# Kernel tuning notes

Measured on AMD Instinct MI355X. Metric: run time of the kernel, lower is better.

## Reference

```python
import jax, jax.numpy as jnp
import numpy as np

EPS = 1e-8


def setup_inputs() -> dict:
    key = jax.random.key(0)
    k1, k2, k3, k4, k5 = jax.random.split(key, 5)
    B, N_LOG, N_PHYS, E = 16, 512, 2048, 2048
    P = jax.random.uniform(k1, (B, N_LOG, N_PHYS), dtype=jnp.float32)
    d_hw = jax.random.randint(k2, (N_PHYS, N_PHYS), 0, 4, dtype=jnp.int32)
    edge_src = jax.random.randint(k3, (B, E), 0, N_LOG, dtype=jnp.int32)
    edge_dst = jax.random.randint(k4, (B, E), 0, N_LOG, dtype=jnp.int32)
    edge_w = jax.random.uniform(k5, (B, E), dtype=jnp.float32)
    return {"P": P, "d_hw": d_hw, "edge_src": edge_src,
            "edge_dst": edge_dst, "edge_w": edge_w}


def reference(P, d_hw, edge_src, edge_dst, edge_w):
    # A_hw[p,q] = 1 where hardware distance == 1 (adjacent qubits)
    A_hw = (d_hw == 1).astype(P.dtype)                      # [Q, Q]
    B = P.shape[0]
    # Dense contraction once per batch: PA[b,i,q] = sum_p P[b,i,p] A[p,q]
    PA = jnp.einsum('bip,pq->biq', P, A_hw)                 # [B, N, Q]
    b_idx = jnp.arange(B)[:, None]                          # [B, 1]
    gi = PA[b_idx, edge_src]                                # [B, E, Q]
    gj = P[b_idx, edge_dst]                                 # [B, E, Q]
    adj_score = jnp.einsum('beq,beq->be', gi, gj)           # [B, E]
    sample_adj = jnp.sum(edge_w * adj_score, axis=-1)       # [B]
    sample_weight = jnp.maximum(jnp.sum(edge_w, axis=-1), EPS)
    # every sample has edges -> valid_samples = B
    loss = -jnp.mean(sample_adj / sample_weight)
    return loss
```

## Files before the change

kernel.cpp:

```cpp
#include <hip/hip_runtime.h>
#include <hip/hip_bf16.h>

#define BATCH 16
#define NLOG 512
#define Q 2048
#define NEDGE 2048
#define M_TOT (BATCH * NLOG)
#define KB 2048

typedef float f32x4 __attribute__((ext_vector_type(4)));
typedef int i32x4 __attribute__((ext_vector_type(4)));
typedef int i32x8 __attribute__((ext_vector_type(8)));

__device__ __forceinline__ unsigned char to_e4m3(float f) {
    int pk = __builtin_amdgcn_cvt_pk_fp8_f32(f, f, 0, false);
    return (unsigned char)(pk & 0xff);
}

__global__ __launch_bounds__(256) void prep(const float* __restrict__ P,
                                            unsigned char* __restrict__ P8,
                                            const int* __restrict__ d_hw,
                                            unsigned char* __restrict__ A8t,
                                            unsigned* __restrict__ counter) {
    int bid = blockIdx.x;
    if (bid == 0 && threadIdx.x == 0) *counter = 0u;
    if (bid < 8192) {
        int i = (bid * 256 + threadIdx.x) * 8;
        float4 v0 = *(const float4*)(P + i);
        float4 v1 = *(const float4*)(P + i + 4);
        int lo = 0, hi = 0;
        lo = __builtin_amdgcn_cvt_pk_fp8_f32(v0.x, v0.y, lo, false);
        lo = __builtin_amdgcn_cvt_pk_fp8_f32(v0.z, v0.w, lo, true);
        hi = __builtin_amdgcn_cvt_pk_fp8_f32(v1.x, v1.y, hi, false);
        hi = __builtin_amdgcn_cvt_pk_fp8_f32(v1.z, v1.w, hi, true);
        int2 st; st.x = lo; st.y = hi;
        *(int2*)(P8 + i) = st;
    } else {
        bid -= 8192;
        __shared__ unsigned char tile[32][33];
        int q0 = (bid & 63) * 32;
        int p0 = (bid >> 6) * 32;
        int tx = threadIdx.x & 31;
        int ty = threadIdx.x >> 5;
        for (int s = 0; s < 32; s += 8) {
            int p = p0 + ty + s;
            int v = d_hw[(size_t)p * Q + q0 + tx];
            tile[ty + s][tx] = (v == 1) ? 0x38 : 0x00;
        }
        __syncthreads();
        for (int s = 0; s < 32; s += 8) {
            A8t[(size_t)(q0 + ty + s) * Q + p0 + tx] = tile[tx][ty + s];
        }
    }
}

__global__ __launch_bounds__(256, 2) void gemm_bt8(const unsigned char* __restrict__ A,
                                                   const unsigned char* __restrict__ Bt,
                                                   unsigned char* __restrict__ PA8) {
    __shared__ unsigned char As[32768];
    __shared__ unsigned char Bs[16384];

    const int t = threadIdx.x;
    const int w = t >> 6;
    const int wr = w >> 1, wc = w & 1;
    const int l = t & 63;
    const int quad = l >> 4;
    const int lane16 = l & 15;

    const int m0 = blockIdx.x * 256;
    const int n0 = blockIdx.y * 128;

    const int s_row = t >> 3;
    const int s_off = (((t & 7) ^ (s_row & 7)) << 4);

    const int r7 = lane16 & 7;
    const int c0 = ((2 * quad) ^ r7) << 4;
    const int c1 = ((2 * quad + 1) ^ r7) << 4;

    f32x4 acc[8][4] = {};

    for (int k0 = 0; k0 < KB; k0 += 128) {
        #pragma unroll
        for (int c = 0; c < 8; c++) {
            const unsigned char* g = A + (size_t)(m0 + c * 32 + s_row) * KB + k0 + s_off;
            __builtin_amdgcn_global_load_lds(
                (const __attribute__((address_space(1))) void*)g,
                (__attribute__((address_space(3))) void*)(As + c * 4096 + w * 1024),
                16, 0, 0);
        }
        #pragma unroll
        for (int c = 0; c < 4; c++) {
            const unsigned char* g = Bt + (size_t)(n0 + c * 32 + s_row) * KB + k0 + s_off;
            __builtin_amdgcn_global_load_lds(
                (const __attribute__((address_space(1))) void*)g,
                (__attribute__((address_space(3))) void*)(Bs + c * 4096 + w * 1024),
                16, 0, 0);
        }
        __syncthreads();

        i32x8 bfr[4];
        #pragma unroll
        for (int j = 0; j < 4; j++) {
            int base = (wc * 64 + j * 16 + lane16) << 7;
            i32x4 lo = *(const i32x4*)(Bs + base + c0);
            i32x4 hi = *(const i32x4*)(Bs + base + c1);
            bfr[j] = __builtin_shufflevector(lo, hi, 0, 1, 2, 3, 4, 5, 6, 7);
        }
        #pragma unroll
        for (int i = 0; i < 8; i++) {
            int base = (wr * 128 + i * 16 + lane16) << 7;
            i32x4 lo = *(const i32x4*)(As + base + c0);
            i32x4 hi = *(const i32x4*)(As + base + c1);
            i32x8 af = __builtin_shufflevector(lo, hi, 0, 1, 2, 3, 4, 5, 6, 7);
            #pragma unroll
            for (int j = 0; j < 4; j++)
                acc[i][j] = __builtin_amdgcn_mfma_scale_f32_16x16x128_f8f6f4(
                    af, bfr[j], acc[i][j], 0, 0,
                    0, 127,
                    0, 127);
        }
        __syncthreads();
    }

    #pragma unroll
    for (int i = 0; i < 8; i++) {
        #pragma unroll
        for (int j = 0; j < 4; j++) {
            #pragma unroll
            for (int r = 0; r < 4; r++) {
                int row = m0 + wr * 128 + i * 16 + quad * 4 + r;
                int col = n0 + wc * 64 + j * 16 + lane16;
                PA8[(size_t)row * Q + col] = to_e4m3(acc[i][j][r] * (1.0f / 256.0f));
            }
        }
    }
}

__global__ __launch_bounds__(256, 2) void gemm_s8(const unsigned char* __restrict__ PA8,
                                                  const unsigned char* __restrict__ P8,
                                                  __hip_bfloat16* __restrict__ S) {
    __shared__ unsigned char As[8192];
    __shared__ unsigned char Bs[16384];

    const int t = threadIdx.x;
    const int w = t >> 6;
    const int wr = w >> 1, wc = w & 1;
    const int l = t & 63;
    const int quad = l >> 4;
    const int lane16 = l & 15;

    const int b = blockIdx.z;
    const int m0 = blockIdx.x * 64;
    const int n0 = blockIdx.y * 128;
    const unsigned char* A  = PA8 + (size_t)b * NLOG * Q;
    const unsigned char* Bt = P8  + (size_t)b * NLOG * Q;
    __hip_bfloat16* C = S + (size_t)b * NLOG * NLOG;

    const int s_row = t >> 3;
    const int s_off = (((t & 7) ^ (s_row & 7)) << 4);
    const int r7 = lane16 & 7;
    const int c0 = ((2 * quad) ^ r7) << 4;
    const int c1 = ((2 * quad + 1) ^ r7) << 4;

    f32x4 acc[2][4] = {};

    for (int k0 = 0; k0 < KB; k0 += 128) {
        #pragma unroll
        for (int c = 0; c < 2; c++) {
            const unsigned char* g = A + (size_t)(m0 + c * 32 + s_row) * KB + k0 + s_off;
            __builtin_amdgcn_global_load_lds(
                (const __attribute__((address_space(1))) void*)g,
                (__attribute__((address_space(3))) void*)(As + c * 4096 + w * 1024),
                16, 0, 0);
        }
        #pragma unroll
        for (int c = 0; c < 4; c++) {
            const unsigned char* g = Bt + (size_t)(n0 + c * 32 + s_row) * KB + k0 + s_off;
            __builtin_amdgcn_global_load_lds(
                (const __attribute__((address_space(1))) void*)g,
                (__attribute__((address_space(3))) void*)(Bs + c * 4096 + w * 1024),
                16, 0, 0);
        }
        __syncthreads();

        i32x8 bfr[4];
        #pragma unroll
        for (int j = 0; j < 4; j++) {
            int base = (wc * 64 + j * 16 + lane16) << 7;
            i32x4 lo = *(const i32x4*)(Bs + base + c0);
            i32x4 hi = *(const i32x4*)(Bs + base + c1);
            bfr[j] = __builtin_shufflevector(lo, hi, 0, 1, 2, 3, 4, 5, 6, 7);
        }
        #pragma unroll
        for (int i = 0; i < 2; i++) {
            int base = (wr * 32 + i * 16 + lane16) << 7;
            i32x4 lo = *(const i32x4*)(As + base + c0);
            i32x4 hi = *(const i32x4*)(As + base + c1);
            i32x8 af = __builtin_shufflevector(lo, hi, 0, 1, 2, 3, 4, 5, 6, 7);
            #pragma unroll
            for (int j = 0; j < 4; j++)
                acc[i][j] = __builtin_amdgcn_mfma_scale_f32_16x16x128_f8f6f4(
                    af, bfr[j], acc[i][j], 0, 0, 0, 127, 0, 127);
        }
        __syncthreads();
    }

    #pragma unroll
    for (int i = 0; i < 2; i++) {
        #pragma unroll
        for (int j = 0; j < 4; j++) {
            #pragma unroll
            for (int r = 0; r < 4; r++) {
                int row = m0 + wr * 32 + i * 16 + quad * 4 + r;
                int col = n0 + wc * 64 + j * 16 + lane16;
                C[(size_t)row * NLOG + col] = __float2bfloat16(acc[i][j][r]);
            }
        }
    }
}

__global__ __launch_bounds__(256) void edge_final(const __hip_bfloat16* __restrict__ S,
                                                  const int* __restrict__ esrc,
                                                  const int* __restrict__ edst,
                                                  const float* __restrict__ ew,
                                                  float* __restrict__ adj,
                                                  float* __restrict__ wsum,
                                                  unsigned* __restrict__ counter,
                                                  float* __restrict__ out) {
    const int b = blockIdx.x;
    const int t = threadIdx.x;
    const unsigned short* Sb = (const unsigned short*)S + (size_t)b * NLOG * NLOG;
    float a = 0.f, ws = 0.f;
    #pragma unroll
    for (int k = 0; k < NEDGE / 256; k++) {
        int e = b * NEDGE + k * 256 + t;
        int src = esrc[e];
        int dst = edst[e];
        float wg = ew[e];
        float s = __uint_as_float((unsigned)Sb[src * NLOG + dst] << 16) * 256.0f;
        a += wg * s;
        ws += wg;
    }
    #pragma unroll
    for (int off = 32; off > 0; off >>= 1) {
        a += __shfl_xor(a, off);
        ws += __shfl_xor(ws, off);
    }
    __shared__ float ra[4], rw[4];
    if ((t & 63) == 0) { ra[t >> 6] = a; rw[t >> 6] = ws; }
    __syncthreads();

    __shared__ unsigned done;
    if (t == 0) {
        atomicExch(&adj[b],  ra[0] + ra[1] + ra[2] + ra[3]);
        atomicExch(&wsum[b], rw[0] + rw[1] + rw[2] + rw[3]);
        __threadfence();
        done = atomicAdd(counter, 1u);
    }
    __syncthreads();
    if (done == BATCH - 1 && t == 0) {
        __threadfence();
        float s = 0.f;
        #pragma unroll
        for (int bb = 0; bb < BATCH; bb++) {
            float av = atomicAdd(&adj[bb], 0.0f);
            float wv = atomicAdd(&wsum[bb], 0.0f);
            s += av / fmaxf(wv, 1e-8f);
        }
        out[0] = -s / (float)BATCH;
    }
}

extern "C" void kernel_launch(void* const* d_in, const int* in_sizes, int n_in,
                              void* d_out, int out_size, void* d_ws, size_t ws_size,
                              hipStream_t stream) {
    const float* P    = (const float*)d_in[0];
    const int* d_hw   = (const int*)d_in[1];
    const int* esrc   = (const int*)d_in[2];
    const int* edst   = (const int*)d_in[3];
    const float* ew   = (const float*)d_in[4];
    float* out        = (float*)d_out;

    char* ws = (char*)d_ws;
    unsigned char* P8  = (unsigned char*)ws;
    unsigned char* A8t = (unsigned char*)(ws + 16777216);
    unsigned char* PA8 = (unsigned char*)(ws + 20971520);
    __hip_bfloat16* S  = (__hip_bfloat16*)(ws + 37748736);
    float* adj         = (float*)(ws + 46137344);
    float* wsum        = (float*)(ws + 46137344 + 64);
    unsigned* counter  = (unsigned*)(ws + 46137344 + 128);

    prep<<<8192 + 4096, 256, 0, stream>>>(P, P8, d_hw, A8t, counter);
    gemm_bt8<<<dim3(M_TOT / 256, Q / 128), 256, 0, stream>>>(P8, A8t, PA8);
    gemm_s8<<<dim3(NLOG / 64, NLOG / 128, BATCH), 256, 0, stream>>>(PA8, P8, S);
    edge_final<<<BATCH, 256, 0, stream>>>(S, esrc, edst, ew, adj, wsum, counter, out);
}
```

Before: 181.4 us.

## Reassociate loss as masked P^T W P contraction with scattered edge weights

Scatters edge weights into a dense per-batch W matrix, computes V = P^T W P over the batch-concatenated K dimension, and reduces V against a bitmask of adjacent hardware pairs. This replaces the P·A GEMM plus per-sample S GEMM and edge gather. The per-sample weight normalization is folded into the gemm1 epilogue. It adds fp8 quantization of W and of the scaled intermediate, which can cost accuracy, and it performs an fp8 transpose of P in prep.

```diff
diff --git a/kernel.cpp b/kernel.cpp
--- a/kernel.cpp
+++ b/kernel.cpp
@@ -5,8 +5,7 @@
 #define NLOG 512
 #define Q 2048
 #define NEDGE 2048
-#define M_TOT (BATCH * NLOG)
-#define KB 2048
+#define KTOT 8192
 
 typedef float f32x4 __attribute__((ext_vector_type(4)));
 typedef int i32x4 __attribute__((ext_vector_type(4)));
@@ -18,45 +17,90 @@
 }
 
 __global__ __launch_bounds__(256) void prep(const float* __restrict__ P,
-                                            unsigned char* __restrict__ P8,
+                                            unsigned char* __restrict__ P8t,
                                             const int* __restrict__ d_hw,
-                                            unsigned char* __restrict__ A8t,
+                                            unsigned* __restrict__ mask,
+                                            const float* __restrict__ ew,
+                                            float* __restrict__ sw,
+                                            float* __restrict__ total,
                                             unsigned* __restrict__ counter) {
+    const int t = threadIdx.x;
     int bid = blockIdx.x;
-    if (bid == 0 && threadIdx.x == 0) *counter = 0u;
-    if (bid < 8192) {
-        int i = (bid * 256 + threadIdx.x) * 8;
-        float4 v0 = *(const float4*)(P + i);
-        float4 v1 = *(const float4*)(P + i + 4);
-        int lo = 0, hi = 0;
-        lo = __builtin_amdgcn_cvt_pk_fp8_f32(v0.x, v0.y, lo, false);
-        lo = __builtin_amdgcn_cvt_pk_fp8_f32(v0.z, v0.w, lo, true);
-        hi = __builtin_amdgcn_cvt_pk_fp8_f32(v1.x, v1.y, hi, false);
-        hi = __builtin_amdgcn_cvt_pk_fp8_f32(v1.z, v1.w, hi, true);
-        int2 st; st.x = lo; st.y = hi;
-        *(int2*)(P8 + i) = st;
+    if (bid < 16384) {
+        __shared__ unsigned char tile[32][36];
+        const int b = bid >> 10;
+        const int tb = bid & 1023;
+        const int i0 = (tb >> 6) * 32;
+        const int p0 = (tb & 63) * 32;
+        const int tx = t & 31, ty = t >> 5;
+        #pragma unroll
+        for (int s = 0; s < 4; s++) {
+            int r = ty + s * 8;
+            float v = P[(size_t)(b * NLOG + i0 + r) * Q + p0 + tx];
+            tile[r][tx] = to_e4m3(v);
+        }
+        __syncthreads();
+        const int r2 = t >> 3;
+        const int c4 = (t & 7) * 4;
+        uchar4 o;
+        o.x = tile[c4 + 0][r2];
+        o.y = tile[c4 + 1][r2];
+        o.z = tile[c4 + 2][r2];
+        o.w = tile[c4 + 3][r2];
+        *(uchar4*)(P8t + (size_t)(p0 + r2) * KTOT + b * NLOG + i0 + c4) = o;
+    } else if (bid < 16896) {
+        int wordid = (bid - 16384) * 256 + t;
+        int p = wordid >> 6;
+        int qw = wordid & 63;
+        unsigned m = 0;
+        #pragma unroll
+        for (int u = 0; u < 32; u++) {
+            int d = d_hw[(size_t)p * Q + qw * 32 + u];
+            m |= (unsigned)(d == 1) << u;
+        }
+        mask[wordid] = m;
     } else {
-        bid -= 8192;
-        __shared__ unsigned char tile[32][33];
-        int q0 = (bid & 63) * 32;
-        int p0 = (bid >> 6) * 32;
-        int tx = threadIdx.x & 31;
-        int ty = threadIdx.x >> 5;
-        for (int s = 0; s < 32; s += 8) {
-            int p = p0 + ty + s;
-            int v = d_hw[(size_t)p * Q + q0 + tx];
-            tile[ty + s][tx] = (v == 1) ? 0x38 : 0x00;
-        }
-        __syncthreads();
-        for (int s = 0; s < 32; s += 8) {
-            A8t[(size_t)(q0 + ty + s) * Q + p0 + tx] = tile[tx][ty + s];
-        }
-    }
-}
-
-__global__ __launch_bounds__(256, 2) void gemm_bt8(const unsigned char* __restrict__ A,
-                                                   const unsigned char* __restrict__ Bt,
-                                                   unsigned char* __restrict__ PA8) {
+        int b = bid - 16896;
+        if (b == 0 && t == 0) { *total = 0.f; *counter = 0u; }
+        float s = 0.f;
+        #pragma unroll
+        for (int k = 0; k < 8; k++) s += ew[b * NEDGE + k * 256 + t];
+        #pragma unroll
+        for (int off = 32; off > 0; off >>= 1) s += __shfl_xor(s, off);
+        __shared__ float red[4];
+        if ((t & 63) == 0) red[t >> 6] = s;
+        __syncthreads();
+        if (t == 0) sw[b] = red[0] + red[1] + red[2] + red[3];
+    }
+}
+
+__global__ __launch_bounds__(256) void scatter_w(const int* __restrict__ esrc,
+                                                 const int* __restrict__ edst,
+                                                 const float* __restrict__ ew,
+                                                 float* __restrict__ Wf32) {
+    const int b = blockIdx.x;
+    const int t = threadIdx.x;
+    #pragma unroll
+    for (int s = 0; s < 8; s++) {
+        int e = b * NEDGE + s * 256 + t;
+        atomicAdd(&Wf32[(size_t)b * NLOG * NLOG + esrc[e] * NLOG + edst[e]], ew[e]);
+    }
+}
+
+__global__ __launch_bounds__(256) void cvt_w(const float* __restrict__ Wf32,
+                                             unsigned char* __restrict__ W8) {
+    int i = (blockIdx.x * 256 + threadIdx.x) * 4;
+    float4 v = *(const float4*)(Wf32 + i);
+    int pk = 0;
+    pk = __builtin_amdgcn_cvt_pk_fp8_f32(v.x, v.y, pk, false);
+    pk = __builtin_amdgcn_cvt_pk_fp8_f32(v.z, v.w, pk, true);
+    *(int*)(W8 + i) = pk;
+}
+
+__global__ __launch_bounds__(256, 2) void gemm1(const unsigned char* __restrict__ P8t,
+                                                const unsigned char* __restrict__ W8,
+                                                const float* __restrict__ sw,
+                                                unsigned char* __restrict__ Vt) {
     __shared__ unsigned char As[32768];
     __shared__ unsigned char Bs[16384];
 
@@ -67,22 +111,25 @@
     const int quad = l >> 4;
     const int lane16 = l & 15;
 
+    const int b = blockIdx.z;
     const int m0 = blockIdx.x * 256;
     const int n0 = blockIdx.y * 128;
 
     const int s_row = t >> 3;
     const int s_off = (((t & 7) ^ (s_row & 7)) << 4);
-
     const int r7 = lane16 & 7;
     const int c0 = ((2 * quad) ^ r7) << 4;
     const int c1 = ((2 * quad + 1) ^ r7) << 4;
 
+    const unsigned char* Wb = W8 + (size_t)b * NLOG * NLOG;
+
     f32x4 acc[8][4] = {};
 
-    for (int k0 = 0; k0 < KB; k0 += 128) {
+    for (int k0 = 0; k0 < NLOG; k0 += 128) {
         #pragma unroll
         for (int c = 0; c < 8; c++) {
-            const unsigned char* g = A + (size_t)(m0 + c * 32 + s_row) * KB + k0 + s_off;
+            const unsigned char* g = P8t + (size_t)(m0 + c * 32 + s_row) * KTOT
+                                     + b * NLOG + k0 + s_off;
             __builtin_amdgcn_global_load_lds(
                 (const __attribute__((address_space(1))) void*)g,
                 (__attribute__((address_space(3))) void*)(As + c * 4096 + w * 1024),
@@ -90,7 +137,8 @@
         }
         #pragma unroll
         for (int c = 0; c < 4; c++) {
-            const unsigned char* g = Bt + (size_t)(n0 + c * 32 + s_row) * KB + k0 + s_off;
+            const unsigned char* g = Wb + (size_t)(n0 + c * 32 + s_row) * NLOG
+                                     + k0 + s_off;
             __builtin_amdgcn_global_load_lds(
                 (const __attribute__((address_space(1))) void*)g,
                 (__attribute__((address_space(3))) void*)(Bs + c * 4096 + w * 1024),
@@ -115,31 +163,41 @@
             #pragma unroll
             for (int j = 0; j < 4; j++)
                 acc[i][j] = __builtin_amdgcn_mfma_scale_f32_16x16x128_f8f6f4(
-                    af, bfr[j], acc[i][j], 0, 0,
-                    0, 127,
-                    0, 127);
-        }
-        __syncthreads();
-    }
-
-    #pragma unroll
-    for (int i = 0; i < 8; i++) {
-        #pragma unroll
-        for (int j = 0; j < 4; j++) {
+                    af, bfr[j], acc[i][j], 0, 0, 0, 127, 0, 127);
+        }
+        __syncthreads();
+    }
+
+    const float scale = 1024.0f / fmaxf(sw[b], 1e-8f);
+    unsigned char* Cs = As;
+    #pragma unroll
+    for (int i = 0; i < 8; i++)
+        #pragma unroll
+        for (int j = 0; j < 4; j++)
             #pragma unroll
             for (int r = 0; r < 4; r++) {
-                int row = m0 + wr * 128 + i * 16 + quad * 4 + r;
-                int col = n0 + wc * 64 + j * 16 + lane16;
-                PA8[(size_t)row * Q + col] = to_e4m3(acc[i][j][r] * (1.0f / 256.0f));
+                int row = wr * 128 + i * 16 + quad * 4 + r;
+                int col = wc * 64 + j * 16 + lane16;
+                Cs[row * 128 + col] = to_e4m3(acc[i][j][r] * scale);
             }
-        }
-    }
-}
-
-__global__ __launch_bounds__(256, 2) void gemm_s8(const unsigned char* __restrict__ PA8,
-                                                  const unsigned char* __restrict__ P8,
-                                                  __hip_bfloat16* __restrict__ S) {
-    __shared__ unsigned char As[8192];
+    __syncthreads();
+    #pragma unroll
+    for (int s = 0; s < 8; s++) {
+        int idx = s * 4096 + t * 16;
+        int row = idx >> 7;
+        int col = idx & 127;
+        *(i32x4*)(Vt + (size_t)(m0 + row) * KTOT + b * NLOG + n0 + col) =
+            *(const i32x4*)(Cs + idx);
+    }
+}
+
+__global__ __launch_bounds__(256, 2) void gemm2(const unsigned char* __restrict__ P8t,
+                                                const unsigned char* __restrict__ Vt,
+                                                const unsigned* __restrict__ mask,
+                                                float* __restrict__ total,
+                                                unsigned* __restrict__ counter,
+                                                float* __restrict__ out) {
+    __shared__ unsigned char As[32768];
     __shared__ unsigned char Bs[16384];
 
     const int t = threadIdx.x;
@@ -149,12 +207,9 @@
     const int quad = l >> 4;
     const int lane16 = l & 15;
 
-    const int b = blockIdx.z;
-    const int m0 = blockIdx.x * 64;
+    const int m0 = blockIdx.x * 256;
     const int n0 = blockIdx.y * 128;
-    const unsigned char* A  = PA8 + (size_t)b * NLOG * Q;
-    const unsigned char* Bt = P8  + (size_t)b * NLOG * Q;
-    __hip_bfloat16* C = S + (size_t)b * NLOG * NLOG;
+    const int kbase = blockIdx.z * 2048;
 
     const int s_row = t >> 3;
     const int s_off = (((t & 7) ^ (s_row & 7)) << 4);
@@ -162,12 +217,13 @@
     const int c0 = ((2 * quad) ^ r7) << 4;
     const int c1 = ((2 * quad + 1) ^ r7) << 4;
 
-    f32x4 acc[2][4] = {};
-
-    for (int k0 = 0; k0 < KB; k0 += 128) {
-        #pragma unroll
-        for (int c = 0; c < 2; c++) {
-            const unsigned char* g = A + (size_t)(m0 + c * 32 + s_row) * KB + k0 + s_off;
+    f32x4 acc[8][4] = {};
+
+    for (int k0 = 0; k0 < 2048; k0 += 128) {
+        #pragma unroll
+        for (int c = 0; c < 8; c++) {
+            const unsigned char* g = P8t + (size_t)(m0 + c * 32 + s_row) * KTOT
+                                     + kbase + k0 + s_off;
             __builtin_amdgcn_global_load_lds(
                 (const __attribute__((address_space(1))) void*)g,
                 (__attribute__((address_space(3))) void*)(As + c * 4096 + w * 1024),
@@ -175,7 +231,8 @@
         }
         #pragma unroll
         for (int c = 0; c < 4; c++) {
-            const unsigned char* g = Bt + (size_t)(n0 + c * 32 + s_row) * KB + k0 + s_off;
+            const unsigned char* g = Vt + (size_t)(n0 + c * 32 + s_row) * KTOT
+                                     + kbase + k0 + s_off;
             __builtin_amdgcn_global_load_lds(
                 (const __attribute__((address_space(1))) void*)g,
                 (__attribute__((address_space(3))) void*)(Bs + c * 4096 + w * 1024),
@@ -192,8 +249,8 @@
             bfr[j] = __builtin_shufflevector(lo, hi, 0, 1, 2, 3, 4, 5, 6, 7);
         }
         #pragma unroll
-        for (int i = 0; i < 2; i++) {
-            int base = (wr * 32 + i * 16 + lane16) << 7;
+        for (int i = 0; i < 8; i++) {
+            int base = (wr * 128 + i * 16 + lane16) << 7;
             i32x4 lo = *(const i32x4*)(As + base + c0);
             i32x4 hi = *(const i32x4*)(As + base + c1);
             i32x8 af = __builtin_shufflevector(lo, hi, 0, 1, 2, 3, 4, 5, 6, 7);
@@ -205,69 +262,37 @@
         __syncthreads();
     }
 
-    #pragma unroll
-    for (int i = 0; i < 2; i++) {
-        #pragma unroll
-        for (int j = 0; j < 4; j++) {
+    float part = 0.f;
+    #pragma unroll
+    for (int i = 0; i < 8; i++) {
+        #pragma unroll
+        for (int r = 0; r < 4; r++) {
+            int p = m0 + wr * 128 + i * 16 + quad * 4 + r;
             #pragma unroll
-            for (int r = 0; r < 4; r++) {
-                int row = m0 + wr * 32 + i * 16 + quad * 4 + r;
-                int col = n0 + wc * 64 + j * 16 + lane16;
-                C[(size_t)row * NLOG + col] = __float2bfloat16(acc[i][j][r]);
+            for (int j = 0; j < 4; j++) {
+                int q = n0 + wc * 64 + j * 16 + lane16;
+                unsigned mw = mask[p * (Q / 32) + (q >> 5)];
+                if ((mw >> (q & 31)) & 1u) part += acc[i][j][r];
             }
         }
     }
-}
-
-__global__ __launch_bounds__(256) void edge_final(const __hip_bfloat16* __restrict__ S,
-                                                  const int* __restrict__ esrc,
-                                                  const int* __restrict__ edst,
-                                                  const float* __restrict__ ew,
-                                                  float* __restrict__ adj,
-                                                  float* __restrict__ wsum,
-                                                  unsigned* __restrict__ counter,
-                                                  float* __restrict__ out) {
-    const int b = blockIdx.x;
-    const int t = threadIdx.x;
-    const unsigned short* Sb = (const unsigned short*)S + (size_t)b * NLOG * NLOG;
-    float a = 0.f, ws = 0.f;
-    #pragma unroll
-    for (int k = 0; k < NEDGE / 256; k++) {
-        int e = b * NEDGE + k * 256 + t;
-        int src = esrc[e];
-        int dst = edst[e];
-        float wg = ew[e];
-        float s = __uint_as_float((unsigned)Sb[src * NLOG + dst] << 16) * 256.0f;
-        a += wg * s;
-        ws += wg;
-    }
-    #pragma unroll
-    for (int off = 32; off > 0; off >>= 1) {
-        a += __shfl_xor(a, off);
-        ws += __shfl_xor(ws, off);
-    }
-    __shared__ float ra[4], rw[4];
-    if ((t & 63) == 0) { ra[t >> 6] = a; rw[t >> 6] = ws; }
+    #pragma unroll
+    for (int off = 32; off > 0; off >>= 1) part += __shfl_xor(part, off);
+    __shared__ float red[4];
+    if (l == 0) red[w] = part;
     __syncthreads();
 
     __shared__ unsigned done;
     if (t == 0) {
-        atomicExch(&adj[b],  ra[0] + ra[1] + ra[2] + ra[3]);
-        atomicExch(&wsum[b], rw[0] + rw[1] + rw[2] + rw[3]);
+        atomicAdd(total, red[0] + red[1] + red[2] + red[3]);
         __threadfence();
         done = atomicAdd(counter, 1u);
     }
     __syncthreads();
-    if (done == BATCH - 1 && t == 0) {
+    if (t == 0 && done == 8 * 16 * 4 - 1) {
         __threadfence();
-        float s = 0.f;
-        #pragma unroll
-        for (int bb = 0; bb < BATCH; bb++) {
-            float av = atomicAdd(&adj[bb], 0.0f);
-            float wv = atomicAdd(&wsum[bb], 0.0f);
-            s += av / fmaxf(wv, 1e-8f);
-        }
-        out[0] = -s / (float)BATCH;
+        float tv = atomicAdd(total, 0.0f);
+        out[0] = -tv / 16384.0f;
     }
 }
 
@@ -282,16 +307,21 @@
     float* out        = (float*)d_out;
 
     char* ws = (char*)d_ws;
-    unsigned char* P8  = (unsigned char*)ws;
-    unsigned char* A8t = (unsigned char*)(ws + 16777216);
-    unsigned char* PA8 = (unsigned char*)(ws + 20971520);
-    __hip_bfloat16* S  = (__hip_bfloat16*)(ws + 37748736);
-    float* adj         = (float*)(ws + 46137344);
-    float* wsum        = (float*)(ws + 46137344 + 64);
-    unsigned* counter  = (unsigned*)(ws + 46137344 + 128);
-
-    prep<<<8192 + 4096, 256, 0, stream>>>(P, P8, d_hw, A8t, counter);
-    gemm_bt8<<<dim3(M_TOT / 256, Q / 128), 256, 0, stream>>>(P8, A8t, PA8);
-    gemm_s8<<<dim3(NLOG / 64, NLOG / 128, BATCH), 256, 0, stream>>>(PA8, P8, S);
-    edge_final<<<BATCH, 256, 0, stream>>>(S, esrc, edst, ew, adj, wsum, counter, out);
-}
+    unsigned char* P8t = (unsigned char*)ws;
+    unsigned char* W8  = (unsigned char*)(ws + 16777216);
+    float* Wf32        = (float*)(ws + 20971520);
+    unsigned char* Vt  = (unsigned char*)(ws + 20971520);
+    unsigned* mask     = (unsigned*)(ws + 37748736);
+    float* sw          = (float*)(ws + 38273024);
+    float* total       = (float*)(ws + 38273088);
+    unsigned* counter  = (unsigned*)(ws + 38273152);
+
+    hipMemsetAsync(Wf32, 0, 16777216, stream);
+    prep<<<16384 + 512 + 16, 256, 0, stream>>>(P, P8t, d_hw, mask, ew, sw,
+                                               total, counter);
+    scatter_w<<<BATCH, 256, 0, stream>>>(esrc, edst, ew, Wf32);
+    cvt_w<<<4096, 256, 0, stream>>>(Wf32, W8);
+    gemm1<<<dim3(Q / 256, NLOG / 128, BATCH), 256, 0, stream>>>(P8t, W8, sw, Vt);
+    gemm2<<<dim3(Q / 256, Q / 128, 4), 256, 0, stream>>>(P8t, Vt, mask, total,
+                                                         counter, out);
+}
```

After: 188.2 us. 3.7% more time.

## Fuse edge reduction into S GEMM epilogue via scattered dense edge-weight matrix

Applied to the files above, without the earlier changes.

Edge weights are scattered with atomics into a dense per-batch fp32 weight matrix during prep, along with per-batch weight sums. The second GEMM then multiplies its accumulators by the matching weight entries and reduces straight into a global total, so the bf16 S matrix write and the separate edge_final kernel go away. The cost is a 16 MB memset, 16 MB of fp32 weight reads in the GEMM epilogue, and atomics on a single total scalar. It also drops the bf16 rounding of S.

```diff
diff --git a/kernel.cpp b/kernel.cpp
--- a/kernel.cpp
+++ b/kernel.cpp
@@ -21,11 +21,17 @@
                                             unsigned char* __restrict__ P8,
                                             const int* __restrict__ d_hw,
                                             unsigned char* __restrict__ A8t,
+                                            const int* __restrict__ esrc,
+                                            const int* __restrict__ edst,
+                                            const float* __restrict__ ew,
+                                            float* __restrict__ Wf32,
+                                            float* __restrict__ sw,
+                                            float* __restrict__ total,
                                             unsigned* __restrict__ counter) {
+    const int t = threadIdx.x;
     int bid = blockIdx.x;
-    if (bid == 0 && threadIdx.x == 0) *counter = 0u;
     if (bid < 8192) {
-        int i = (bid * 256 + threadIdx.x) * 8;
+        int i = (bid * 256 + t) * 8;
         float4 v0 = *(const float4*)(P + i);
         float4 v1 = *(const float4*)(P + i + 4);
         int lo = 0, hi = 0;
@@ -35,13 +41,13 @@
         hi = __builtin_amdgcn_cvt_pk_fp8_f32(v1.z, v1.w, hi, true);
         int2 st; st.x = lo; st.y = hi;
         *(int2*)(P8 + i) = st;
-    } else {
+    } else if (bid < 12288) {
         bid -= 8192;
         __shared__ unsigned char tile[32][33];
         int q0 = (bid & 63) * 32;
         int p0 = (bid >> 6) * 32;
-        int tx = threadIdx.x & 31;
-        int ty = threadIdx.x >> 5;
+        int tx = t & 31;
+        int ty = t >> 5;
         for (int s = 0; s < 32; s += 8) {
             int p = p0 + ty + s;
             int v = d_hw[(size_t)p * Q + q0 + tx];
@@ -51,6 +57,24 @@
         for (int s = 0; s < 32; s += 8) {
             A8t[(size_t)(q0 + ty + s) * Q + p0 + tx] = tile[tx][ty + s];
         }
+    } else {
+        int b = bid - 12288;
+        if (b == 0 && t == 0) { *total = 0.f; *counter = 0u; }
+        float s = 0.f;
+        float* Wb = Wf32 + (size_t)b * NLOG * NLOG;
+        #pragma unroll
+        for (int k = 0; k < 8; k++) {
+            int e = b * NEDGE + k * 256 + t;
+            float wg = ew[e];
+            s += wg;
+            atomicAdd(&Wb[esrc[e] * NLOG + edst[e]], wg);
+        }
+        #pragma unroll
+        for (int off = 32; off > 0; off >>= 1) s += __shfl_xor(s, off);
+        __shared__ float red[4];
+        if ((t & 63) == 0) red[t >> 6] = s;
+        __syncthreads();
+        if (t == 0) sw[b] = red[0] + red[1] + red[2] + red[3];
     }
 }
 
@@ -72,7 +96,6 @@
 
     const int s_row = t >> 3;
     const int s_off = (((t & 7) ^ (s_row & 7)) << 4);
-
     const int r7 = lane16 & 7;
     const int c0 = ((2 * quad) ^ r7) << 4;
     const int c1 = ((2 * quad + 1) ^ r7) << 4;
@@ -115,9 +138,7 @@
             #pragma unroll
             for (int j = 0; j < 4; j++)
                 acc[i][j] = __builtin_amdgcn_mfma_scale_f32_16x16x128_f8f6f4(
-                    af, bfr[j], acc[i][j], 0, 0,
-                    0, 127,
-                    0, 127);
+                    af, bfr[j], acc[i][j], 0, 0, 0, 127, 0, 127);
         }
         __syncthreads();
     }
@@ -136,9 +157,13 @@
     }
 }
 
-__global__ __launch_bounds__(256, 2) void gemm_s8(const unsigned char* __restrict__ PA8,
+__global__ __launch_bounds__(256, 2) void gemm_sw(const unsigned char* __restrict__ PA8,
                                                   const unsigned char* __restrict__ P8,
-                                                  __hip_bfloat16* __restrict__ S) {
+                                                  const float* __restrict__ Wf32,
+                                                  const float* __restrict__ sw,
+                                                  float* __restrict__ total,
+                                                  unsigned* __restrict__ counter,
+                                                  float* __restrict__ out) {
     __shared__ unsigned char As[8192];
     __shared__ unsigned char Bs[16384];
 
@@ -154,7 +179,7 @@
     const int n0 = blockIdx.y * 128;
     const unsigned char* A  = PA8 + (size_t)b * NLOG * Q;
     const unsigned char* Bt = P8  + (size_t)b * NLOG * Q;
-    __hip_bfloat16* C = S + (size_t)b * NLOG * NLOG;
+    const float* Wb = Wf32 + (size_t)b * NLOG * NLOG;
 
     const int s_row = t >> 3;
     const int s_off = (((t & 7) ^ (s_row & 7)) << 4);
@@ -205,69 +230,35 @@
         __syncthreads();
     }
 
+    float part = 0.f;
     #pragma unroll
     for (int i = 0; i < 2; i++) {
         #pragma unroll
-        for (int j = 0; j < 4; j++) {
-            #pragma unroll
-            for (int r = 0; r < 4; r++) {
-                int row = m0 + wr * 32 + i * 16 + quad * 4 + r;
-                int col = n0 + wc * 64 + j * 16 + lane16;
-                C[(size_t)row * NLOG + col] = __float2bfloat16(acc[i][j][r]);
-            }
-        }
-    }
-}
-
-__global__ __launch_bounds__(256) void edge_final(const __hip_bfloat16* __restrict__ S,
-                                                  const int* __restrict__ esrc,
-                                                  const int* __restrict__ edst,
-                                                  const float* __restrict__ ew,
-                                                  float* __restrict__ adj,
-                                                  float* __restrict__ wsum,
-                                                  unsigned* __restrict__ counter,
-                                                  float* __restrict__ out) {
-    const int b = blockIdx.x;
-    const int t = threadIdx.x;
-    const unsigned short* Sb = (const unsigned short*)S + (size_t)b * NLOG * NLOG;
-    float a = 0.f, ws = 0.f;
+        for (int r = 0; r < 4; r++) {
+            int row = m0 + wr * 32 + i * 16 + quad * 4 + r;
+            const float* wrow = Wb + (size_t)row * NLOG + n0 + wc * 64 + lane16;
+            #pragma unroll
+            for (int j = 0; j < 4; j++)
+                part += wrow[j * 16] * acc[i][j][r];
+        }
+    }
     #pragma unroll
-    for (int k = 0; k < NEDGE / 256; k++) {
-        int e = b * NEDGE + k * 256 + t;
-        int src = esrc[e];
-        int dst = edst[e];
-        float wg = ew[e];
-        float s = __uint_as_float((unsigned)Sb[src * NLOG + dst] << 16) * 256.0f;
-        a += wg * s;
-        ws += wg;
-    }
-    #pragma unroll
-    for (int off = 32; off > 0; off >>= 1) {
-        a += __shfl_xor(a, off);
-        ws += __shfl_xor(ws, off);
-    }
-    __shared__ float ra[4], rw[4];
-    if ((t & 63) == 0) { ra[t >> 6] = a; rw[t >> 6] = ws; }
+    for (int off = 32; off > 0; off >>= 1) part += __shfl_xor(part, off);
+    __shared__ float red[4];
+    if (l == 0) red[w] = part;
     __syncthreads();
 
     __shared__ unsigned done;
     if (t == 0) {
-        atomicExch(&adj[b],  ra[0] + ra[1] + ra[2] + ra[3]);
-        atomicExch(&wsum[b], rw[0] + rw[1] + rw[2] + rw[3]);
+        float scale = 256.0f / (16.0f * fmaxf(sw[b], 1e-8f));
+        atomicAdd(total, (red[0] + red[1] + red[2] + red[3]) * scale);
         __threadfence();
         done = atomicAdd(counter, 1u);
     }
     __syncthreads();
-    if (done == BATCH - 1 && t == 0) {
+    if (t == 0 && done == 512 - 1) {
         __threadfence();
-        float s = 0.f;
-        #pragma unroll
-        for (int bb = 0; bb < BATCH; bb++) {
-            float av = atomicAdd(&adj[bb], 0.0f);
-            float wv = atomicAdd(&wsum[bb], 0.0f);
-            s += av / fmaxf(wv, 1e-8f);
-        }
-        out[0] = -s / (float)BATCH;
+        out[0] = -atomicAdd(total, 0.0f);
     }
 }
 
@@ -285,13 +276,15 @@
     unsigned char* P8  = (unsigned char*)ws;
     unsigned char* A8t = (unsigned char*)(ws + 16777216);
     unsigned char* PA8 = (unsigned char*)(ws + 20971520);
-    __hip_bfloat16* S  = (__hip_bfloat16*)(ws + 37748736);
-    float* adj         = (float*)(ws + 46137344);
-    float* wsum        = (float*)(ws + 46137344 + 64);
-    unsigned* counter  = (unsigned*)(ws + 46137344 + 128);
-
-    prep<<<8192 + 4096, 256, 0, stream>>>(P, P8, d_hw, A8t, counter);
+    float* Wf32        = (float*)(ws + 37748736);
+    float* sw          = (float*)(ws + 54525952);
+    float* total       = (float*)(ws + 54525952 + 64);
+    unsigned* counter  = (unsigned*)(ws + 54525952 + 128);
+
+    hipMemsetAsync(Wf32, 0, 16777216, stream);
+    prep<<<8192 + 4096 + 16, 256, 0, stream>>>(P, P8, d_hw, A8t, esrc, edst, ew,
+                                               Wf32, sw, total, counter);
     gemm_bt8<<<dim3(M_TOT / 256, Q / 128), 256, 0, stream>>>(P8, A8t, PA8);
-    gemm_s8<<<dim3(NLOG / 64, NLOG / 128, BATCH), 256, 0, stream>>>(PA8, P8, S);
-    edge_final<<<BATCH, 256, 0, stream>>>(S, esrc, edst, ew, adj, wsum, counter, out);
-}
+    gemm_sw<<<dim3(NLOG / 64, NLOG / 128, BATCH), 256, 0, stream>>>(
+        PA8, P8, Wf32, sw, total, counter, out);
+}
```

Result: slower. 192.0 us (+5.8%).
